# Kernel optimization log

Measured on AMD Instinct MI355X. Metric: run time of the kernel, lower is better.

The kernel has to match this reference:

```python
import jax, jax.numpy as jnp
import numpy as np

D_EMBED = 1024
N_HEADS = 16


def setup_inputs() -> dict:
    key = jax.random.key(0)
    ks = jax.random.split(key, 5)
    x = jax.random.normal(ks[0], (4, 2048, D_EMBED), dtype=jnp.float32)
    # fused QKV projection: Linear(d, 3d)
    w_qkv = jax.random.normal(ks[1], (D_EMBED, 3 * D_EMBED), dtype=jnp.float32) / np.sqrt(D_EMBED)
    b_qkv = jnp.zeros((3 * D_EMBED,), dtype=jnp.float32)
    # output projection: Linear(d, d)
    w_o = jax.random.normal(ks[2], (D_EMBED, D_EMBED), dtype=jnp.float32) / np.sqrt(D_EMBED)
    b_o = jnp.zeros((D_EMBED,), dtype=jnp.float32)
    return {"x": x, "w_qkv": w_qkv, "b_qkv": b_qkv, "w_o": w_o, "b_o": b_o}


def reference(x, w_qkv, b_qkv, w_o, b_o):
    bs, sl, ed = x.shape
    nh = N_HEADS
    hd = ed // nh
    qkv = x @ w_qkv + b_qkv                      # [bs, sl, 3*ed]
    q, k, v = jnp.split(qkv, 3, axis=-1)
    # (bs, sl, nh*hd) -> (bs, nh, sl, hd)
    q = q.reshape(bs, sl, nh, hd).transpose(0, 2, 1, 3)
    k = k.reshape(bs, sl, nh, hd).transpose(0, 2, 1, 3)
    v = v.reshape(bs, sl, nh, hd).transpose(0, 2, 1, 3)
    att = jnp.einsum('bhqd,bhkd->bhqk', q, k) * (1.0 / np.sqrt(hd))
    causal = jnp.tril(jnp.ones((sl, sl), dtype=bool))
    att = jnp.where(causal[None, None], att, jnp.float32(-jnp.inf))
    att = jax.nn.softmax(att, axis=-1)
    y = jnp.einsum('bhqk,bhkd->bhqd', att, v)    # [bs, nh, sl, hd]
    y = y.transpose(0, 2, 1, 3).reshape(bs, sl, ed)
    return y @ w_o + b_o
```

## Files before the change

### kernel.cpp

```cpp
#include <hip/hip_runtime.h>
#include <hip/hip_bf16.h>
#include <stdint.h>

typedef __attribute__((ext_vector_type(8))) __bf16 bf16x8;
typedef __attribute__((ext_vector_type(4))) __bf16 bf16x4;
typedef __attribute__((ext_vector_type(4))) float f32x4;

#define MFMA16(a, b, c) __builtin_amdgcn_mfma_f32_16x16x32_bf16((a), (b), (c), 0, 0, 0)

static __device__ __forceinline__ void gload_lds16(const void* g, void* l) {
  __builtin_amdgcn_global_load_lds(
      reinterpret_cast<const __attribute__((address_space(1))) uint32_t*>(
          reinterpret_cast<uintptr_t>(g)),
      reinterpret_cast<__attribute__((address_space(3))) uint32_t*>(
          reinterpret_cast<uintptr_t>(l)),
      16, 0, 0);
}

__global__ void cvt_f32_bf16(const float* __restrict__ in, __bf16* __restrict__ out, int n) {
  int i = (blockIdx.x * blockDim.x + threadIdx.x) * 8;
  if (i >= n) return;
  float4 a = *(const float4*)(in + i);
  float4 b = *(const float4*)(in + i + 4);
  bf16x8 o;
  o[0] = (__bf16)a.x; o[1] = (__bf16)a.y; o[2] = (__bf16)a.z; o[3] = (__bf16)a.w;
  o[4] = (__bf16)b.x; o[5] = (__bf16)b.y; o[6] = (__bf16)b.z; o[7] = (__bf16)b.w;
  *(bf16x8*)(out + i) = o;
}

__global__ void transpose_cvt(const float* __restrict__ in, __bf16* __restrict__ out,
                              int R, int C) {
  __shared__ float tile[32][33];
  int c0 = blockIdx.x * 32, r0 = blockIdx.y * 32;
  int tx = threadIdx.x, ty = threadIdx.y;
#pragma unroll
  for (int i = 0; i < 4; i++)
    tile[ty + i * 8][tx] = in[(size_t)(r0 + ty + i * 8) * C + c0 + tx];
  __syncthreads();
#pragma unroll
  for (int i = 0; i < 4; i++)
    out[(size_t)(c0 + ty + i * 8) * R + r0 + tx] = (__bf16)tile[tx][ty + i * 8];
}

template <int EPI>
__global__ __launch_bounds__(512) void gemm_pipe(
    const __bf16* __restrict__ A, const __bf16* __restrict__ Bt,
    const float* __restrict__ bias, float* __restrict__ Cf,
    __bf16* __restrict__ Qb, __bf16* __restrict__ Kb, __bf16* __restrict__ Vtb, int N) {
  __shared__ __bf16 lA[3][128 * 32];
  __shared__ __bf16 lB[3][256 * 32];
  const int bid0 = (int)(blockIdx.y * gridDim.x + blockIdx.x);
  const int tM = (bid0 & 7) * 8 + ((bid0 >> 3) & 7);
  const int tN = bid0 >> 6;
  const int tid = threadIdx.x;
  const int w = tid >> 6, lane = tid & 63;
  const int wr = w >> 2, wc = w & 3;
  const int lr = lane & 15, lg = lane >> 4;

  const int srow = tid >> 2;
  const int gcol = ((tid & 3) ^ ((tid >> 3) & 3)) * 8;
  const __bf16* Asrc = A + (size_t)(tM * 128 + srow) * 1024 + gcol;
  const __bf16* Bsrc0 = Bt + (size_t)(tN * 256 + srow) * 1024 + gcol;
  const __bf16* Bsrc1 = Bt + (size_t)(tN * 256 + 128 + srow) * 1024 + gcol;

  f32x4 acc[4][4];
#pragma unroll
  for (int m = 0; m < 4; m++)
#pragma unroll
    for (int n = 0; n < 4; n++) acc[m][n] = f32x4{0.f, 0.f, 0.f, 0.f};

  auto stage = [&](int slot, int t) {
    const int k0 = t * 32;
    gload_lds16(Asrc + k0, &lA[slot][tid * 8]);
    gload_lds16(Bsrc0 + k0, &lB[slot][tid * 8]);
    gload_lds16(Bsrc1 + k0, &lB[slot][4096 + tid * 8]);
  };

  const int aslot = (lg ^ ((lr >> 1) & 3)) * 8;
  auto compute = [&](int slot) {
    bf16x8 a[4], b[4];
#pragma unroll
    for (int m = 0; m < 4; m++) {
      int row = wr * 64 + m * 16 + lr;
      a[m] = *(const bf16x8*)&lA[slot][row * 32 + aslot];
    }
#pragma unroll
    for (int n = 0; n < 4; n++) {
      int row = wc * 64 + n * 16 + lr;
      b[n] = *(const bf16x8*)&lB[slot][row * 32 + aslot];
    }
    __builtin_amdgcn_s_setprio(1);
#pragma unroll
    for (int m = 0; m < 4; m++)
#pragma unroll
      for (int n = 0; n < 4; n++) acc[m][n] = MFMA16(a[m], b[n], acc[m][n]);
    __builtin_amdgcn_s_setprio(0);
  };

  stage(0, 0); stage(1, 1);
  asm volatile("s_waitcnt vmcnt(3)" ::: "memory");
  __builtin_amdgcn_s_barrier();

#pragma unroll 1
  for (int t = 0; t < 30; ++t) {
    stage((t + 2) % 3, t + 2);
    compute(t % 3);
    asm volatile("s_waitcnt vmcnt(3)" ::: "memory");
    __builtin_amdgcn_s_barrier();
  }
  compute(30 % 3);
  asm volatile("s_waitcnt vmcnt(0)" ::: "memory");
  __builtin_amdgcn_s_barrier();
  compute(31 % 3);

#pragma unroll
  for (int m = 0; m < 4; m++) {
#pragma unroll
    for (int n = 0; n < 4; n++) {
      int row0 = tM * 128 + wr * 64 + m * 16 + lg * 4;
      int col = tN * 256 + wc * 64 + n * 16 + lr;
      float bv = bias[col];
      if (EPI == 0) {
        int which = col >> 10, rem = col & 1023;
        int hh = rem >> 6, dd = rem & 63;
        if (which == 2) {
#pragma unroll
          for (int r = 0; r < 4; r++) {
            int row = row0 + r;
            int b = row >> 11, s = row & 2047;
            Vtb[((size_t)(b * 16 + hh) * 64 + dd) * 2048 + s] = (__bf16)(acc[m][n][r] + bv);
          }
        } else {
          __bf16* dst = (which == 0) ? Qb : Kb;
          float sc = (which == 0) ? 0.18033688f : 1.0f;
#pragma unroll
          for (int r = 0; r < 4; r++) {
            int row = row0 + r;
            int b = row >> 11, s = row & 2047;
            dst[((size_t)(b * 16 + hh) * 2048 + s) * 64 + dd] = (__bf16)((acc[m][n][r] + bv) * sc);
          }
        }
      } else {
#pragma unroll
        for (int r = 0; r < 4; r++)
          Cf[(size_t)(row0 + r) * N + col] = acc[m][n][r] + bv;
      }
    }
  }
}

__global__ __launch_bounds__(256) void attn_fwd(
    const __bf16* __restrict__ Q, const __bf16* __restrict__ K,
    const __bf16* __restrict__ Vt, __bf16* __restrict__ Y) {
  const int pair = blockIdx.y;
  const int bh = blockIdx.x;
  const int w = threadIdx.x >> 6, lane = threadIdx.x & 63;
  const int lr = lane & 15, lg = lane >> 4;
  const int b = bh >> 4, h = bh & 15;
  const __bf16* Qp = Q + (size_t)bh * 131072;
  const __bf16* Kp = K + (size_t)bh * 131072;
  const __bf16* Vp = Vt + (size_t)bh * 131072;

  __shared__ __bf16 Kl[4][4096];
  __shared__ __bf16 Vl[4][4096];
  __shared__ __bf16 Pl[4][32 * 64];
  __bf16* Pw = Pl[w];

  bf16x8 kones;
#pragma unroll
  for (int j = 0; j < 8; j++) kones[j] = (__bf16)1.0f;

  auto stage = [&](int slot, int t_) {
    const int kv0_ = t_ * 64;
#pragma unroll
    for (int is = 0; is < 2; is++) {
      int rr = w * 16 + is * 8 + (lane >> 3);
      int sc = ((lane & 7) ^ (rr & 7)) * 8;
      gload_lds16(Kp + (size_t)(kv0_ + rr) * 64 + sc, &Kl[slot][(w * 16 + is * 8) * 64]);
      gload_lds16(Vp + (size_t)rr * 2048 + kv0_ + sc, &Vl[slot][(w * 16 + is * 8) * 64]);
    }
  };

  for (int sel = 0; sel < 2; ++sel) {
    const int qt = sel ? (15 - pair) : pair;
    const int qbase = qt * 128 + w * 32;

    bf16x8 aq[2][2];
#pragma unroll
    for (int m = 0; m < 2; m++)
#pragma unroll
      for (int c = 0; c < 2; c++)
        aq[m][c] = *(const bf16x8*)&Qp[(size_t)(qbase + m * 16 + lr) * 64 + c * 32 + lg * 8];

    f32x4 acc_o[2][4];
    f32x4 acc_l[2];
#pragma unroll
    for (int m = 0; m < 2; m++) {
#pragma unroll
      for (int dn = 0; dn < 4; dn++) acc_o[m][dn] = f32x4{0.f, 0.f, 0.f, 0.f};
      acc_l[m] = f32x4{0.f, 0.f, 0.f, 0.f};
    }

    const int nt = 2 * qt + 2;

    stage(0, 0);
    stage(1, 1);

#pragma unroll 1
    for (int t = 0; t < nt; ++t) {
      const int kv0 = t * 64;
      if (t + 2 < nt) stage((t + 2) & 3, t + 2);

      if (t + 2 < nt) {
        asm volatile("s_waitcnt vmcnt(8)" ::: "memory");
      } else if (t + 1 < nt) {
        asm volatile("s_waitcnt vmcnt(4)" ::: "memory");
      } else {
        asm volatile("s_waitcnt vmcnt(0)" ::: "memory");
      }
      __builtin_amdgcn_s_barrier();

      if (kv0 <= qbase + 31) {
        const int cur = t & 3;
        f32x4 s4[2][4];
#pragma unroll
        for (int m = 0; m < 2; m++)
#pragma unroll
          for (int n = 0; n < 4; n++) s4[m][n] = f32x4{0.f, 0.f, 0.f, 0.f};
        __builtin_amdgcn_s_setprio(1);
#pragma unroll
        for (int c = 0; c < 2; c++) {
#pragma unroll
          for (int n = 0; n < 4; n++) {
            int kr = n * 16 + lr;
            int off = kr * 64 + (((c * 64 + lg * 16) ^ ((kr & 7) << 4)) >> 1);
            bf16x8 bk = *(const bf16x8*)&Kl[cur][off];
#pragma unroll
            for (int m = 0; m < 2; m++) s4[m][n] = MFMA16(bk, aq[m][c], s4[m][n]);
          }
        }
        __builtin_amdgcn_s_setprio(0);

        const bool diag = (kv0 + 63 > qbase);
#pragma unroll
        for (int m = 0; m < 2; m++) {
          const int qrow = qbase + m * 16 + lr;
          if (diag) {
#pragma unroll
            for (int n = 0; n < 4; n++)
#pragma unroll
              for (int r = 0; r < 4; r++)
                if (kv0 + n * 16 + lg * 4 + r > qrow) s4[m][n][r] = -1e30f;
          }
#pragma unroll
          for (int n = 0; n < 4; n++) {
            bf16x4 pq;
#pragma unroll
            for (int r = 0; r < 4; r++)
              pq[r] = (__bf16)__builtin_amdgcn_exp2f(s4[m][n][r] - 16.0f);
            int off = (m * 16 + lr) * 64 + (((n * 32 + lg * 8) ^ ((lr & 7) << 4)) >> 1);
            *(bf16x4*)&Pw[off] = pq;
          }
        }

        bf16x8 ap[2][2];
#pragma unroll
        for (int m = 0; m < 2; m++)
#pragma unroll
          for (int cc = 0; cc < 2; cc++) {
            int off = (m * 16 + lr) * 64 + (((cc * 64 + lg * 16) ^ ((lr & 7) << 4)) >> 1);
            ap[m][cc] = *(const bf16x8*)&Pw[off];
          }

        __builtin_amdgcn_s_setprio(1);
#pragma unroll
        for (int m = 0; m < 2; m++)
#pragma unroll
          for (int cc = 0; cc < 2; cc++)
            acc_l[m] = MFMA16(ap[m][cc], kones, acc_l[m]);
#pragma unroll
        for (int dn = 0; dn < 4; dn++) {
          int d = dn * 16 + lr;
#pragma unroll
          for (int cc = 0; cc < 2; cc++) {
            int off = d * 64 + (((cc * 64 + lg * 16) ^ ((d & 7) << 4)) >> 1);
            bf16x8 bv = *(const bf16x8*)&Vl[cur][off];
#pragma unroll
            for (int m = 0; m < 2; m++) acc_o[m][dn] = MFMA16(ap[m][cc], bv, acc_o[m][dn]);
          }
        }
        __builtin_amdgcn_s_setprio(0);
      }
    }

    __syncthreads();

#pragma unroll
    for (int m = 0; m < 2; m++) {
#pragma unroll
      for (int r = 0; r < 4; r++) {
        float iv = 1.f / acc_l[m][r];
        int row = b * 2048 + qbase + m * 16 + lg * 4 + r;
#pragma unroll
        for (int dn = 0; dn < 4; dn++)
          Y[(size_t)row * 1024 + h * 64 + dn * 16 + lr] = (__bf16)(acc_o[m][dn][r] * iv);
      }
    }
  }
}

extern "C" void kernel_launch(void* const* d_in, const int* in_sizes, int n_in,
                              void* d_out, int out_size, void* d_ws, size_t ws_size,
                              hipStream_t stream) {
  const float* x = (const float*)d_in[0];
  const float* wqkv = (const float*)d_in[1];
  const float* bqkv = (const float*)d_in[2];
  const float* wo = (const float*)d_in[3];
  const float* bo = (const float*)d_in[4];
  float* out = (float*)d_out;

  __bf16* ws = (__bf16*)d_ws;
  __bf16* xb = ws;
  __bf16* wqkvT = xb + 8388608;
  __bf16* woT = wqkvT + 3145728;
  __bf16* Qb = woT + 1048576;
  __bf16* Kb = Qb + 8388608;
  __bf16* Vtb = Kb + 8388608;
  __bf16* Yb = xb;

  cvt_f32_bf16<<<4096, 256, 0, stream>>>(x, xb, 8388608);
  dim3 tb(32, 8);
  transpose_cvt<<<dim3(96, 32), tb, 0, stream>>>(wqkv, wqkvT, 1024, 3072);
  transpose_cvt<<<dim3(32, 32), tb, 0, stream>>>(wo, woT, 1024, 1024);
  gemm_pipe<0><<<dim3(64, 12), 512, 0, stream>>>(xb, wqkvT, bqkv, nullptr, Qb, Kb, Vtb, 3072);
  attn_fwd<<<dim3(64, 8), 256, 0, stream>>>(Qb, Kb, Vtb, Yb);
  gemm_pipe<1><<<dim3(64, 4), 512, 0, stream>>>(Yb, woT, bo, out, nullptr, nullptr, nullptr, 1024);
}
```

Before: 168.8 us.

## Enlarge GEMM tiles to 256x256 with split-K-half double-buffered pipelined schedule

The GEMM kernel moves from a 128x256 tile with a triple-buffered 32-wide K pipeline to a 256x256 tile. The new tile is double-buffered over a 64-wide K step, and each step is split into four MFMA phases that interleave LDS fragment reads and async global-to-LDS staging with barriers. This is meant to raise arithmetic intensity and overlap loads with MFMA work. In exchange, LDS and register use per block grow and block counts shrink, leaving only 128 blocks for the output projection, which may underfill the GPU.

```diff
diff --git a/kernel.cpp b/kernel.cpp
--- a/kernel.cpp
+++ b/kernel.cpp
@@ -47,77 +47,126 @@
     const __bf16* __restrict__ A, const __bf16* __restrict__ Bt,
     const float* __restrict__ bias, float* __restrict__ Cf,
     __bf16* __restrict__ Qb, __bf16* __restrict__ Kb, __bf16* __restrict__ Vtb, int N) {
-  __shared__ __bf16 lA[3][128 * 32];
-  __shared__ __bf16 lB[3][256 * 32];
-  const int bid0 = (int)(blockIdx.y * gridDim.x + blockIdx.x);
-  const int tM = (bid0 & 7) * 8 + ((bid0 >> 3) & 7);
-  const int tN = bid0 >> 6;
+  __shared__ __bf16 lA[32768];
+  __shared__ __bf16 lB[32768];
+  const int bx = (int)blockIdx.x;
+  const int idx = bx >> 3;
+  const int tM = (bx & 7) * 4 + (idx & 3);
+  const int tN = idx >> 2;
   const int tid = threadIdx.x;
   const int w = tid >> 6, lane = tid & 63;
   const int wr = w >> 2, wc = w & 3;
   const int lr = lane & 15, lg = lane >> 4;
 
-  const int srow = tid >> 2;
-  const int gcol = ((tid & 3) ^ ((tid >> 3) & 3)) * 8;
-  const __bf16* Asrc = A + (size_t)(tM * 128 + srow) * 1024 + gcol;
-  const __bf16* Bsrc0 = Bt + (size_t)(tN * 256 + srow) * 1024 + gcol;
-  const __bf16* Bsrc1 = Bt + (size_t)(tN * 256 + 128 + srow) * 1024 + gcol;
-
-  f32x4 acc[4][4];
-#pragma unroll
-  for (int m = 0; m < 4; m++)
+  const int srow = w * 16 + (lane >> 2);
+  const int gk8 = ((lane & 3) ^ ((lane >> 3) & 3)) * 8;
+  const __bf16* Abase = A + (size_t)(tM * 256 + srow) * 1024 + gk8;
+  const __bf16* Bbase = Bt + (size_t)(tN * 256 + srow) * 1024 + gk8;
+
+  auto stageA = [&](int buf, int kh, int t) {
+    const int k0 = t * 64 + kh * 32;
+    __bf16* d = &lA[(buf * 2 + kh) * 8192 + w * 512];
+    gload_lds16(Abase + k0, d);
+    gload_lds16(Abase + 128 * 1024 + k0, d + 4096);
+  };
+  auto stageB = [&](int buf, int kh, int t) {
+    const int k0 = t * 64 + kh * 32;
+    __bf16* d = &lB[(buf * 2 + kh) * 8192 + w * 512];
+    gload_lds16(Bbase + k0, d);
+    gload_lds16(Bbase + 128 * 1024 + k0, d + 4096);
+  };
+
+  const int fslot = (lg ^ ((lr >> 1) & 3)) * 8;
+  auto readA = [&](int buf, int ks, int m) -> bf16x8 {
+    int row = wr * 128 + m * 16 + lr;
+    return *(const bf16x8*)&lA[(buf * 2 + ks) * 8192 + row * 32 + fslot];
+  };
+  auto readB = [&](int buf, int ks, int n) -> bf16x8 {
+    int row = wc * 64 + n * 16 + lr;
+    return *(const bf16x8*)&lB[(buf * 2 + ks) * 8192 + row * 32 + fslot];
+  };
+
+  f32x4 acc[8][4];
+#pragma unroll
+  for (int m = 0; m < 8; m++)
 #pragma unroll
     for (int n = 0; n < 4; n++) acc[m][n] = f32x4{0.f, 0.f, 0.f, 0.f};
 
-  auto stage = [&](int slot, int t) {
-    const int k0 = t * 32;
-    gload_lds16(Asrc + k0, &lA[slot][tid * 8]);
-    gload_lds16(Bsrc0 + k0, &lB[slot][tid * 8]);
-    gload_lds16(Bsrc1 + k0, &lB[slot][4096 + tid * 8]);
-  };
-
-  const int aslot = (lg ^ ((lr >> 1) & 3)) * 8;
-  auto compute = [&](int slot) {
-    bf16x8 a[4], b[4];
-#pragma unroll
-    for (int m = 0; m < 4; m++) {
-      int row = wr * 64 + m * 16 + lr;
-      a[m] = *(const bf16x8*)&lA[slot][row * 32 + aslot];
-    }
+  stageB(0, 0, 0); stageA(0, 0, 0); stageB(0, 1, 0); stageA(0, 1, 0);
+  stageB(1, 0, 1); stageA(1, 0, 1); stageB(1, 1, 1);
+  asm volatile("s_waitcnt vmcnt(6)" ::: "memory");
+  __builtin_amdgcn_s_barrier();
+
+  bf16x8 am[4], bk0[4], bk1[4];
+#pragma unroll 1
+  for (int t = 0; t < 16; ++t) {
+    const int buf = t & 1;
+#pragma unroll
+    for (int m = 0; m < 4; m++) am[m] = readA(buf, 0, m);
+#pragma unroll
+    for (int n = 0; n < 4; n++) bk0[n] = readB(buf, 0, n);
+    if (t + 1 < 16) stageA(buf ^ 1, 1, t + 1);
+    __builtin_amdgcn_s_barrier();
+    asm volatile("s_waitcnt lgkmcnt(0)" ::: "memory");
+    __builtin_amdgcn_s_setprio(1);
+#pragma unroll
+    for (int m = 0; m < 4; m++)
+#pragma unroll
+      for (int n = 0; n < 4; n++) acc[m][n] = MFMA16(am[m], bk0[n], acc[m][n]);
+    __builtin_amdgcn_s_setprio(0);
+    __builtin_amdgcn_s_barrier();
+#pragma unroll
+    for (int m = 0; m < 4; m++) am[m] = readA(buf, 0, m + 4);
+    if (t + 2 < 16) stageB(buf, 0, t + 2);
+    __builtin_amdgcn_s_barrier();
+    asm volatile("s_waitcnt lgkmcnt(0)" ::: "memory");
+    __builtin_amdgcn_s_setprio(1);
+#pragma unroll
+    for (int m = 0; m < 4; m++)
+#pragma unroll
+      for (int n = 0; n < 4; n++) acc[m + 4][n] = MFMA16(am[m], bk0[n], acc[m + 4][n]);
+    __builtin_amdgcn_s_setprio(0);
+    __builtin_amdgcn_s_barrier();
+#pragma unroll
+    for (int m = 0; m < 4; m++) am[m] = readA(buf, 1, m);
+#pragma unroll
+    for (int n = 0; n < 4; n++) bk1[n] = readB(buf, 1, n);
+    if (t + 2 < 16) stageA(buf, 0, t + 2);
+    __builtin_amdgcn_s_barrier();
+    asm volatile("s_waitcnt lgkmcnt(0)" ::: "memory");
+    __builtin_amdgcn_s_setprio(1);
+#pragma unroll
+    for (int m = 0; m < 4; m++)
+#pragma unroll
+      for (int n = 0; n < 4; n++) acc[m][n] = MFMA16(am[m], bk1[n], acc[m][n]);
+    __builtin_amdgcn_s_setprio(0);
+    __builtin_amdgcn_s_barrier();
+#pragma unroll
+    for (int m = 0; m < 4; m++) am[m] = readA(buf, 1, m + 4);
+    if (t + 2 < 16) stageB(buf, 1, t + 2);
+    __builtin_amdgcn_s_barrier();
+    asm volatile("s_waitcnt lgkmcnt(0)" ::: "memory");
+    __builtin_amdgcn_s_setprio(1);
+#pragma unroll
+    for (int m = 0; m < 4; m++)
+#pragma unroll
+      for (int n = 0; n < 4; n++) acc[m + 4][n] = MFMA16(am[m], bk1[n], acc[m + 4][n]);
+    __builtin_amdgcn_s_setprio(0);
+    if (t + 1 < 16) {
+      if (t + 2 < 16) {
+        asm volatile("s_waitcnt vmcnt(6)" ::: "memory");
+      } else {
+        asm volatile("s_waitcnt vmcnt(0)" ::: "memory");
+      }
+    }
+    __builtin_amdgcn_s_barrier();
+  }
+
+#pragma unroll
+  for (int m = 0; m < 8; m++) {
 #pragma unroll
     for (int n = 0; n < 4; n++) {
-      int row = wc * 64 + n * 16 + lr;
-      b[n] = *(const bf16x8*)&lB[slot][row * 32 + aslot];
-    }
-    __builtin_amdgcn_s_setprio(1);
-#pragma unroll
-    for (int m = 0; m < 4; m++)
-#pragma unroll
-      for (int n = 0; n < 4; n++) acc[m][n] = MFMA16(a[m], b[n], acc[m][n]);
-    __builtin_amdgcn_s_setprio(0);
-  };
-
-  stage(0, 0); stage(1, 1);
-  asm volatile("s_waitcnt vmcnt(3)" ::: "memory");
-  __builtin_amdgcn_s_barrier();
-
-#pragma unroll 1
-  for (int t = 0; t < 30; ++t) {
-    stage((t + 2) % 3, t + 2);
-    compute(t % 3);
-    asm volatile("s_waitcnt vmcnt(3)" ::: "memory");
-    __builtin_amdgcn_s_barrier();
-  }
-  compute(30 % 3);
-  asm volatile("s_waitcnt vmcnt(0)" ::: "memory");
-  __builtin_amdgcn_s_barrier();
-  compute(31 % 3);
-
-#pragma unroll
-  for (int m = 0; m < 4; m++) {
-#pragma unroll
-    for (int n = 0; n < 4; n++) {
-      int row0 = tM * 128 + wr * 64 + m * 16 + lg * 4;
+      int row0 = tM * 256 + wr * 128 + m * 16 + lg * 4;
       int col = tN * 256 + wc * 64 + n * 16 + lr;
       float bv = bias[col];
       if (EPI == 0) {
@@ -332,7 +381,7 @@
   dim3 tb(32, 8);
   transpose_cvt<<<dim3(96, 32), tb, 0, stream>>>(wqkv, wqkvT, 1024, 3072);
   transpose_cvt<<<dim3(32, 32), tb, 0, stream>>>(wo, woT, 1024, 1024);
-  gemm_pipe<0><<<dim3(64, 12), 512, 0, stream>>>(xb, wqkvT, bqkv, nullptr, Qb, Kb, Vtb, 3072);
+  gemm_pipe<0><<<384, 512, 0, stream>>>(xb, wqkvT, bqkv, nullptr, Qb, Kb, Vtb, 3072);
   attn_fwd<<<dim3(64, 8), 256, 0, stream>>>(Qb, Kb, Vtb, Yb);
-  gemm_pipe<1><<<dim3(64, 4), 512, 0, stream>>>(Yb, woT, bo, out, nullptr, nullptr, nullptr, 1024);
-}
+  gemm_pipe<1><<<128, 512, 0, stream>>>(Yb, woT, bo, out, nullptr, nullptr, nullptr, 1024);
+}
```

Result: slower. 194.2 us (+15.1%).

## Replace triple-buffered 128x256 GEMM with single-buffered 128x128 tile kernel

Applied to the files above, without the earlier changes.

Swaps the 512-thread, 128x256-tile GEMM that used a 3-stage global-to-LDS pipeline and XOR-swizzled LDS layout for a 256-thread, 128x128-tile kernel. The new kernel loads one K-slice into a single buffer, syncs, computes and syncs again. The block grid doubles, which gives more blocks per GPU and lower LDS use per block. In exchange it loses load/compute overlap and the swizzle, so LDS bank conflicts and exposed memory latency become likely.

```diff
diff --git a/kernel.cpp b/kernel.cpp
--- a/kernel.cpp
+++ b/kernel.cpp
@@ -43,25 +43,27 @@
 }
 
 template <int EPI>
-__global__ __launch_bounds__(512) void gemm_pipe(
+__global__ __launch_bounds__(256) void gemm_bt(
     const __bf16* __restrict__ A, const __bf16* __restrict__ Bt,
     const float* __restrict__ bias, float* __restrict__ Cf,
     __bf16* __restrict__ Qb, __bf16* __restrict__ Kb, __bf16* __restrict__ Vtb, int N) {
-  __shared__ __bf16 lA[3][128 * 32];
-  __shared__ __bf16 lB[3][256 * 32];
+  __shared__ __bf16 lA[128 * 32];
+  __shared__ __bf16 lB[128 * 32];
   const int bid0 = (int)(blockIdx.y * gridDim.x + blockIdx.x);
-  const int tM = (bid0 & 7) * 8 + ((bid0 >> 3) & 7);
-  const int tN = bid0 >> 6;
+  const int j = bid0 >> 3;
+  const int tM = (bid0 & 7) * 8 + (j & 7);
+  const int tN = j >> 3;
   const int tid = threadIdx.x;
   const int w = tid >> 6, lane = tid & 63;
-  const int wr = w >> 2, wc = w & 3;
+  const int wr = w >> 1, wc = w & 1;
   const int lr = lane & 15, lg = lane >> 4;
 
-  const int srow = tid >> 2;
-  const int gcol = ((tid & 3) ^ ((tid >> 3) & 3)) * 8;
-  const __bf16* Asrc = A + (size_t)(tM * 128 + srow) * 1024 + gcol;
-  const __bf16* Bsrc0 = Bt + (size_t)(tN * 256 + srow) * 1024 + gcol;
-  const __bf16* Bsrc1 = Bt + (size_t)(tN * 256 + 128 + srow) * 1024 + gcol;
+  const __bf16* As0 = A + (size_t)(tM * 128 + w * 16 + (lane >> 2)) * 1024 + (lane & 3) * 8;
+  const __bf16* Bs0 = Bt + (size_t)(tN * 128 + w * 16 + (lane >> 2)) * 1024 + (lane & 3) * 8;
+  __bf16* lA0 = &lA[w * 512];
+  __bf16* lA1 = &lA[w * 512 + 2048];
+  __bf16* lB0 = &lB[w * 512];
+  __bf16* lB1 = &lB[w * 512 + 2048];
 
   f32x4 acc[4][4];
 #pragma unroll
@@ -69,56 +71,35 @@
 #pragma unroll
     for (int n = 0; n < 4; n++) acc[m][n] = f32x4{0.f, 0.f, 0.f, 0.f};
 
-  auto stage = [&](int slot, int t) {
-    const int k0 = t * 32;
-    gload_lds16(Asrc + k0, &lA[slot][tid * 8]);
-    gload_lds16(Bsrc0 + k0, &lB[slot][tid * 8]);
-    gload_lds16(Bsrc1 + k0, &lB[slot][4096 + tid * 8]);
-  };
-
-  const int aslot = (lg ^ ((lr >> 1) & 3)) * 8;
-  auto compute = [&](int slot) {
-    bf16x8 a[4], b[4];
-#pragma unroll
-    for (int m = 0; m < 4; m++) {
-      int row = wr * 64 + m * 16 + lr;
-      a[m] = *(const bf16x8*)&lA[slot][row * 32 + aslot];
-    }
-#pragma unroll
-    for (int n = 0; n < 4; n++) {
-      int row = wc * 64 + n * 16 + lr;
-      b[n] = *(const bf16x8*)&lB[slot][row * 32 + aslot];
-    }
+#pragma unroll 1
+  for (int k0 = 0; k0 < 1024; k0 += 32) {
+    gload_lds16(As0 + k0, lA0);
+    gload_lds16(As0 + 64 * 1024 + k0, lA1);
+    gload_lds16(Bs0 + k0, lB0);
+    gload_lds16(Bs0 + 64 * 1024 + k0, lB1);
+    __syncthreads();
+    bf16x8 af[4], bfr[4];
+#pragma unroll
+    for (int m = 0; m < 4; m++)
+      af[m] = *(const bf16x8*)&lA[(wr * 64 + m * 16 + lr) * 32 + lg * 8];
+#pragma unroll
+    for (int n = 0; n < 4; n++)
+      bfr[n] = *(const bf16x8*)&lB[(wc * 64 + n * 16 + lr) * 32 + lg * 8];
     __builtin_amdgcn_s_setprio(1);
 #pragma unroll
     for (int m = 0; m < 4; m++)
 #pragma unroll
-      for (int n = 0; n < 4; n++) acc[m][n] = MFMA16(a[m], b[n], acc[m][n]);
+      for (int n = 0; n < 4; n++) acc[m][n] = MFMA16(af[m], bfr[n], acc[m][n]);
     __builtin_amdgcn_s_setprio(0);
-  };
-
-  stage(0, 0); stage(1, 1);
-  asm volatile("s_waitcnt vmcnt(3)" ::: "memory");
-  __builtin_amdgcn_s_barrier();
-
-#pragma unroll 1
-  for (int t = 0; t < 30; ++t) {
-    stage((t + 2) % 3, t + 2);
-    compute(t % 3);
-    asm volatile("s_waitcnt vmcnt(3)" ::: "memory");
-    __builtin_amdgcn_s_barrier();
+    __syncthreads();
   }
-  compute(30 % 3);
-  asm volatile("s_waitcnt vmcnt(0)" ::: "memory");
-  __builtin_amdgcn_s_barrier();
-  compute(31 % 3);
 
 #pragma unroll
   for (int m = 0; m < 4; m++) {
 #pragma unroll
     for (int n = 0; n < 4; n++) {
       int row0 = tM * 128 + wr * 64 + m * 16 + lg * 4;
-      int col = tN * 256 + wc * 64 + n * 16 + lr;
+      int col = tN * 128 + wc * 64 + n * 16 + lr;
       float bv = bias[col];
       if (EPI == 0) {
         int which = col >> 10, rem = col & 1023;
@@ -332,7 +313,7 @@
   dim3 tb(32, 8);
   transpose_cvt<<<dim3(96, 32), tb, 0, stream>>>(wqkv, wqkvT, 1024, 3072);
   transpose_cvt<<<dim3(32, 32), tb, 0, stream>>>(wo, woT, 1024, 1024);
-  gemm_pipe<0><<<dim3(64, 12), 512, 0, stream>>>(xb, wqkvT, bqkv, nullptr, Qb, Kb, Vtb, 3072);
+  gemm_bt<0><<<dim3(64, 24), 256, 0, stream>>>(xb, wqkvT, bqkv, nullptr, Qb, Kb, Vtb, 3072);
   attn_fwd<<<dim3(64, 8), 256, 0, stream>>>(Qb, Kb, Vtb, Yb);
-  gemm_pipe<1><<<dim3(64, 4), 512, 0, stream>>>(Yb, woT, bo, out, nullptr, nullptr, nullptr, 1024);
-}
+  gemm_bt<1><<<dim3(64, 8), 256, 0, stream>>>(Yb, woT, bo, out, nullptr, nullptr, nullptr, 1024);
+}
```

New measurement: 181.5 us. 1.08x slower.
